# Kernel tuning notes

Hardware: AMD Instinct MI355X
Metric: run time of the kernel (lower is better)

Reference implementation:

```python
import jax, jax.numpy as jnp
import numpy as np

D_MODEL, D_K, D_V, HEAD = 512, 512, 512, 8
SCALE = 1.0 / np.sqrt(D_K)  # torch code divides by sqrt(d_k) (full d_k, not head_dim)
NEG = -1.0e9


def setup_inputs() -> dict:
    key = jax.random.key(0)
    ks = jax.random.split(key, 10)
    B, S = 2, 4096
    x = jax.random.normal(ks[0], (B, S, D_MODEL), dtype=jnp.float32)
    mask = jax.random.randint(ks[1], (B, S), 0, 2, dtype=jnp.int32)
    s = 1.0 / np.sqrt(D_MODEL)
    Wq = jax.random.normal(ks[2], (D_MODEL, D_K), dtype=jnp.float32) * s
    bq = jnp.zeros((D_K,), jnp.float32)
    Wk = jax.random.normal(ks[3], (D_MODEL, D_K), dtype=jnp.float32) * s
    bk = jnp.zeros((D_K,), jnp.float32)
    Wv = jax.random.normal(ks[4], (D_MODEL, D_V), dtype=jnp.float32) * s
    bv = jnp.zeros((D_V,), jnp.float32)
    Wo = jax.random.normal(ks[5], (D_V, D_MODEL), dtype=jnp.float32) * s
    bo = jnp.zeros((D_MODEL,), jnp.float32)
    return {"x": x, "mask": mask, "Wq": Wq, "bq": bq, "Wk": Wk, "bk": bk,
            "Wv": Wv, "bv": bv, "Wo": Wo, "bo": bo}


def reference(x, mask, Wq, bq, Wk, bk, Wv, bv, Wo, bo):
    B, S, _ = x.shape
    hd_k = D_K // HEAD
    hd_v = D_V // HEAD
    # projections -> [B, H, S, hd]
    Q = (x @ Wq + bq).reshape(B, S, HEAD, hd_k).transpose(0, 2, 1, 3)
    K = (x @ Wk + bk).reshape(B, S, HEAD, hd_k).transpose(0, 2, 1, 3)
    V = (x @ Wv + bv).reshape(B, S, HEAD, hd_v).transpose(0, 2, 1, 3)
    # scores [B, H, S, S], scaled by 1/sqrt(d_k) (full d_k, faithful to source)
    scores = jnp.einsum('bhqd,bhkd->bhqk', Q, K) * SCALE
    m = (mask == 1)[:, None, None, :]  # [B,1,1,S]
    scores = jnp.where(m, NEG, scores)
    attn = jax.nn.softmax(scores, axis=-1)
    out = jnp.einsum('bhqk,bhkd->bhqd', attn, V)  # [B,H,S,hd_v]
    out = out.transpose(0, 2, 1, 3).reshape(B, S, D_V)
    return out @ Wo + bo
```

## Files before the change

kernel.cpp:

```cpp
#include <hip/hip_runtime.h>
#include <hip/hip_bf16.h>
#include <stdint.h>

typedef __attribute__((ext_vector_type(8))) short bf16x8;
typedef __attribute__((ext_vector_type(4))) float f32x4;
typedef __attribute__((ext_vector_type(16))) float f32x16;
typedef __attribute__((ext_vector_type(4))) unsigned int u32x4;

#define MFMA16(a, b, c) __builtin_amdgcn_mfma_f32_16x16x32_bf16(a, b, c, 0, 0, 0)
#define MFMA32(a, b, c) __builtin_amdgcn_mfma_f32_32x32x16_bf16(a, b, c, 0, 0, 0)

constexpr float QSCALE = 0.04419417382415922f * 1.4426950408889634f;

__device__ __forceinline__ void gload_lds16(const void* g, void* l) {
  __builtin_amdgcn_global_load_lds((const __attribute__((address_space(1))) uint32_t*)g,
                                   (__attribute__((address_space(3))) uint32_t*)l, 16, 0, 0);
}
__device__ __forceinline__ bf16x8 lds_read_swz(const short* base, int row, int ch) {
  return *(const bf16x8*)((const char*)base + row * 128 + (((ch ^ row) & 7) << 4));
}
__device__ __forceinline__ short f2b(float f) {
  __hip_bfloat16 h = __float2bfloat16(f);
  return *reinterpret_cast<short*>(&h);
}
__device__ __forceinline__ float exp2fast(float x) {
#if __has_builtin(__builtin_amdgcn_exp2f)
  return __builtin_amdgcn_exp2f(x);
#else
  return exp2f(x);
#endif
}

__global__ void k_cvt_x(const float* __restrict__ x, short* __restrict__ xb) {
  const int i = blockIdx.x * 256 + threadIdx.x;
  const float4 v = ((const float4*)x)[i];
  short4 o;
  o.x = f2b(v.x); o.y = f2b(v.y); o.z = f2b(v.z); o.w = f2b(v.w);
  ((short4*)xb)[i] = o;
}

__global__ void k_cvt_w(const float* __restrict__ wq, const float* __restrict__ wk,
                        const float* __restrict__ wv, const float* __restrict__ wo,
                        short* __restrict__ wt) {
  __shared__ float tile[64][65];
  const int mat = blockIdx.x >> 6;
  const int t6 = blockIdx.x & 63;
  const int k0 = (t6 >> 3) * 64, n0 = (t6 & 7) * 64;
  const float* w = (mat == 0) ? wq : (mat == 1) ? wk : (mat == 2) ? wv : wo;
  const int c = threadIdx.x & 63, r4 = threadIdx.x >> 6;
#pragma unroll
  for (int p = 0; p < 16; ++p) {
    const int r = p * 4 + r4;
    tile[r][c] = w[(k0 + r) * 512 + n0 + c];
  }
  __syncthreads();
#pragma unroll
  for (int p = 0; p < 16; ++p) {
    const int r = p * 4 + r4;
    wt[mat * 262144 + (n0 + r) * 512 + k0 + c] = f2b(tile[c][r]);
  }
}

__global__ void k_scan(const int* __restrict__ mask, int* __restrict__ perm,
                       int* __restrict__ cnt) {
  __shared__ int ws[16];
  const int b = blockIdx.x, tid = threadIdx.x;
  const int lane = tid & 63, w = tid >> 6;
  const int* m = mask + b * 4096;
  int v[4], s = 0;
#pragma unroll
  for (int j = 0; j < 4; ++j) { v[j] = (m[tid * 4 + j] == 0) ? 1 : 0; s += v[j]; }
  int sc = s;
  for (int d = 1; d < 64; d <<= 1) { int t = __shfl_up(sc, d); if (lane >= d) sc += t; }
  if (lane == 63) ws[w] = sc;
  __syncthreads();
  if (tid == 0) {
    int acc = 0;
    for (int i = 0; i < 16; ++i) { int t = ws[i]; ws[i] = acc; acc += t; }
    cnt[b] = acc;
  }
  __syncthreads();
  int pos = ws[w] + sc - s;
  int* p = perm + b * 4096;
#pragma unroll
  for (int j = 0; j < 4; ++j) { p[tid * 4 + j] = v[j] ? pos : -1; pos += v[j]; }
}

__global__ __launch_bounds__(256, 2) void k_gemmqkv(
    const short* __restrict__ A, const short* __restrict__ W,
    const float* __restrict__ bq, const float* __restrict__ bk,
    const float* __restrict__ bv, const int* __restrict__ perm,
    short* __restrict__ oq, short* __restrict__ ok, short* __restrict__ ov) {
  __shared__ short Asm[2][128 * 64];
  __shared__ short Bsm[2][128 * 64];
  const int tid = threadIdx.x;
  const int wave = tid >> 6, lane = tid & 63;
  const int lane15 = lane & 15, g = lane >> 4;
  const int wm = wave >> 1, wn = wave & 1;
  const int m0 = blockIdx.x * 128;
  const int n0 = blockIdx.y * 128;

  const char* Ag = (const char*)A + (size_t)m0 * 1024;
  const char* Bg = (const char*)W + (size_t)n0 * 1024;

  f32x4 acc[4][4] = {};

  auto stage = [&](int buf, int kt) {
    const int k0b = kt * 128;
#pragma unroll
    for (int q = 0; q < 4; ++q) {
      int s_ = (wave * 4 + q) * 64 + lane;
      int row = s_ >> 3, ch = s_ & 7;
      gload_lds16(Ag + (size_t)row * 1024 + k0b + (((ch ^ row) & 7) << 4),
                  (char*)&Asm[buf][0] + s_ * 16);
      gload_lds16(Bg + (size_t)row * 1024 + k0b + (((ch ^ row) & 7) << 4),
                  (char*)&Bsm[buf][0] + s_ * 16);
    }
  };

  stage(0, 0);
  asm volatile("s_waitcnt vmcnt(0)" ::: "memory");
  __syncthreads();

  for (int kt = 0; kt < 8; ++kt) {
    const int cur = kt & 1;
    if (kt < 7) stage(cur ^ 1, kt + 1);
#pragma unroll
    for (int kk = 0; kk < 2; ++kk) {
      bf16x8 af[4], bfr[4];
#pragma unroll
      for (int m = 0; m < 4; ++m)
        af[m] = lds_read_swz(&Asm[cur][0], wm * 64 + m * 16 + lane15, kk * 4 + g);
#pragma unroll
      for (int n = 0; n < 4; ++n)
        bfr[n] = lds_read_swz(&Bsm[cur][0], wn * 64 + n * 16 + lane15, kk * 4 + g);
      __builtin_amdgcn_s_setprio(1);
#pragma unroll
      for (int m = 0; m < 4; ++m)
#pragma unroll
        for (int n = 0; n < 4; ++n)
          acc[m][n] = MFMA16(bfr[n], af[m], acc[m][n]);
      __builtin_amdgcn_s_setprio(0);
    }
    asm volatile("s_waitcnt vmcnt(0)" ::: "memory");
    __syncthreads();
  }

  const int mat = blockIdx.y >> 2;
  const float* bptr = (mat == 0) ? bq : (mat == 1) ? bk : bv;
  const int hh = ((n0 & 511) >> 6) + wn;
  const int hb = g >> 1, j4 = (g & 1) * 4;

#pragma unroll
  for (int mf = 0; mf < 4; ++mf) {
    const int rowg = m0 + wm * 64 + mf * 16 + lane15;
    const int b_ = rowg >> 12, sl = rowg & 4095;
    const size_t bh = (size_t)(b_ * 8 + hh);
    int pm_ = 0;
    if (mat != 0) pm_ = perm[b_ * 4096 + sl];
#pragma unroll
    for (int nf = 0; nf < 4; ++nf) {
      const int nn = (n0 & 511) + wn * 64 + nf * 16 + g * 4;
      const float4 b4 = *(const float4*)(bptr + nn);
      const float v0 = acc[mf][nf][0] + b4.x;
      const float v1 = acc[mf][nf][1] + b4.y;
      const float v2 = acc[mf][nf][2] + b4.z;
      const float v3 = acc[mf][nf][3] + b4.w;
      if (mat == 0) {
        short4 s4;
        s4.x = f2b(v0 * QSCALE); s4.y = f2b(v1 * QSCALE);
        s4.z = f2b(v2 * QSCALE); s4.w = f2b(v3 * QSCALE);
        *(short4*)(oq + bh * 262144 +
                   (size_t)(((sl >> 5) * 4 + nf) * 64 + hb * 32 + (sl & 31)) * 8 + j4) = s4;
      } else if (pm_ >= 0) {
        const int t = pm_ >> 6, r = pm_ & 63;
        if (mat == 1) {
          short4 s4;
          s4.x = f2b(v0); s4.y = f2b(v1); s4.z = f2b(v2); s4.w = f2b(v3);
          *(short4*)(ok + bh * 262144 +
                     (size_t)((t * 8 + nf * 2 + (r >> 5)) * 64 + hb * 32 + (r & 31)) * 8 + j4) = s4;
        } else {
          const int mm = (r & ~12) | (((r >> 2) & 1) << 3) | (((r >> 3) & 1) << 2);
          short* base = ov + bh * 262144 +
                        (size_t)((t * 8 + ((mm >> 4) & 3) * 2 + (nf >> 1)) * 64 +
                                 ((mm >> 3) & 1) * 32 + (nf & 1) * 16 + g * 4) * 8 + (mm & 7);
          base[0] = f2b(v0); base[8] = f2b(v1); base[16] = f2b(v2); base[24] = f2b(v3);
        }
      }
    }
  }
}

__global__ __launch_bounds__(256, 2) void k_gemmo(
    const short* __restrict__ A, const short* __restrict__ W,
    const float* __restrict__ bias, float* __restrict__ fo) {
  __shared__ short Asm[2][128 * 64];
  __shared__ short Bsm[2][64 * 64];
  const int tid = threadIdx.x;
  const int wave = tid >> 6, lane = tid & 63;
  const int lane15 = lane & 15, g = lane >> 4;
  const int wm = wave >> 1, wn = wave & 1;
  const int m0 = blockIdx.x * 128;
  const int n0 = blockIdx.y * 64;

  const char* Ag = (const char*)A + (size_t)m0 * 1024;
  const char* Bg = (const char*)W + (size_t)n0 * 1024;

  f32x4 acc[4][2] = {};

  auto stage = [&](int buf, int kt) {
    const int k0b = kt * 128;
#pragma unroll
    for (int q = 0; q < 4; ++q) {
      int s_ = (wave * 4 + q) * 64 + lane;
      int row = s_ >> 3, ch = s_ & 7;
      gload_lds16(Ag + (size_t)row * 1024 + k0b + (((ch ^ row) & 7) << 4),
                  (char*)&Asm[buf][0] + s_ * 16);
    }
#pragma unroll
    for (int q = 0; q < 2; ++q) {
      int s_ = (wave * 2 + q) * 64 + lane;
      int row = s_ >> 3, ch = s_ & 7;
      gload_lds16(Bg + (size_t)row * 1024 + k0b + (((ch ^ row) & 7) << 4),
                  (char*)&Bsm[buf][0] + s_ * 16);
    }
  };

  stage(0, 0);
  asm volatile("s_waitcnt vmcnt(0)" ::: "memory");
  __syncthreads();

  for (int kt = 0; kt < 8; ++kt) {
    const int cur = kt & 1;
    if (kt < 7) stage(cur ^ 1, kt + 1);
#pragma unroll
    for (int kk = 0; kk < 2; ++kk) {
      bf16x8 af[4], bfr[2];
#pragma unroll
      for (int m = 0; m < 4; ++m)
        af[m] = lds_read_swz(&Asm[cur][0], wm * 64 + m * 16 + lane15, kk * 4 + g);
#pragma unroll
      for (int n = 0; n < 2; ++n)
        bfr[n] = lds_read_swz(&Bsm[cur][0], wn * 32 + n * 16 + lane15, kk * 4 + g);
      __builtin_amdgcn_s_setprio(1);
#pragma unroll
      for (int m = 0; m < 4; ++m)
#pragma unroll
        for (int n = 0; n < 2; ++n)
          acc[m][n] = MFMA16(bfr[n], af[m], acc[m][n]);
      __builtin_amdgcn_s_setprio(0);
    }
    asm volatile("s_waitcnt vmcnt(0)" ::: "memory");
    __syncthreads();
  }

#pragma unroll
  for (int mf = 0; mf < 4; ++mf) {
    const int rowg = m0 + wm * 64 + mf * 16 + lane15;
#pragma unroll
    for (int nf = 0; nf < 2; ++nf) {
      const int cb = n0 + wn * 32 + nf * 16 + g * 4;
      const float4 b4 = *(const float4*)(bias + cb);
      float4 o4;
      o4.x = acc[mf][nf][0] + b4.x;
      o4.y = acc[mf][nf][1] + b4.y;
      o4.z = acc[mf][nf][2] + b4.z;
      o4.w = acc[mf][nf][3] + b4.w;
      *(float4*)(fo + (size_t)rowg * 512 + cb) = o4;
    }
  }
}

__global__ __launch_bounds__(256, 2) void k_attn(
    const short* __restrict__ Qp, const short* __restrict__ Kp,
    const short* __restrict__ Vp, const int* __restrict__ cnt,
    short* __restrict__ out) {
  __shared__ short Ks[2][8][512];
  __shared__ short Vs[2][8][512];

  const int tid = threadIdx.x;
  const int wave = tid >> 6, lane = tid & 63;
  const int l31 = lane & 31, h = lane >> 5;
  const int bid = blockIdx.x;
  const int sid = (bid & 7) * 64 + (bid >> 3);
  const int qt = sid & 31, bh = sid >> 5;
  const int b = bh >> 3, hh = bh & 7;
  const int qb = qt * 4 + wave;

  const short* Qg = Qp + (size_t)bh * 262144;
  const short* Kg = Kp + (size_t)bh * 262144;
  const short* Vg = Vp + (size_t)bh * 262144;

  bf16x8 qreg[4];
#pragma unroll
  for (int dk = 0; dk < 4; ++dk)
    qreg[dk] = *(const bf16x8*)(Qg + ((size_t)(qb * 4 + dk) * 64 + lane) * 8);

  const int cn = cnt[b];
  const int nt = max(1, (cn + 63) >> 6);
  const int lim = cn - (nt - 1) * 64;

  auto stage = [&](int buf, int t) {
#pragma unroll
    for (int q = 0; q < 2; ++q) {
      const int u = wave * 2 + q;
      gload_lds16(Kg + ((size_t)(t * 8 + u) * 64 + lane) * 8, &Ks[buf][u][lane * 8]);
      gload_lds16(Vg + ((size_t)(t * 8 + u) * 64 + lane) * 8, &Vs[buf][u][lane * 8]);
    }
  };
  auto ldsK = [&](int buf, int u) { return *(const bf16x8*)&Ks[buf][u][lane * 8]; };
  auto ldsV = [&](int buf, int u) { return *(const bf16x8*)&Vs[buf][u][lane * 8]; };

  f32x16 o0 = {}, o1 = {};
  float l_ = 0.f;

  stage(0, 0);
  __syncthreads();

  for (int t = 0; t < nt; ++t) {
    const int cur = t & 1;
    if (t + 1 < nt) stage(cur ^ 1, t + 1);

    f32x16 s0v = {}, s1v = {};
    __builtin_amdgcn_s_setprio(1);
#pragma unroll
    for (int dk = 0; dk < 4; ++dk) {
      s0v = MFMA32(ldsK(cur, 2 * dk), qreg[dk], s0v);
      s1v = MFMA32(ldsK(cur, 2 * dk + 1), qreg[dk], s1v);
    }
    __builtin_amdgcn_s_setprio(0);

    if (t == nt - 1 && lim < 64) {
#pragma unroll
      for (int i = 0; i < 16; ++i) {
        const int r0 = (i & 3) + 8 * (i >> 2) + 4 * h;
        if (r0 >= lim) s0v[i] = -1e30f;
        if (r0 + 32 >= lim) s1v[i] = -1e30f;
      }
    }

    unsigned int wA[8], wB[8];
    float ts = 0.f;
#pragma unroll
    for (int j2 = 0; j2 < 8; ++j2) {
      float a0 = exp2fast(s0v[2 * j2]);
      float a1 = exp2fast(s0v[2 * j2 + 1]);
      float b0 = exp2fast(s1v[2 * j2]);
      float b1 = exp2fast(s1v[2 * j2 + 1]);
      ts += (a0 + a1) + (b0 + b1);
      asm("v_cvt_pk_bf16_f32 %0, %1, %2" : "=v"(wA[j2]) : "v"(a0), "v"(a1));
      asm("v_cvt_pk_bf16_f32 %0, %1, %2" : "=v"(wB[j2]) : "v"(b0), "v"(b1));
    }
    l_ += ts;

    __builtin_amdgcn_s_setprio(1);
#pragma unroll
    for (int s = 0; s < 4; ++s) {
      const bf16x8 v0 = ldsV(cur, 2 * s);
      const bf16x8 v1 = ldsV(cur, 2 * s + 1);
      const unsigned int* w = (s < 2) ? wA : wB;
      union PU { u32x4 u; bf16x8 f; } pu;
      pu.u[0] = w[4 * (s & 1) + 0];
      pu.u[1] = w[4 * (s & 1) + 1];
      pu.u[2] = w[4 * (s & 1) + 2];
      pu.u[3] = w[4 * (s & 1) + 3];
      o0 = MFMA32(v0, pu.f, o0);
      o1 = MFMA32(v1, pu.f, o1);
    }
    __builtin_amdgcn_s_setprio(0);

    __syncthreads();
  }

  l_ += __shfl_xor(l_, 32);
  const float inv = 1.0f / l_;
  short* og = out + (size_t)(b * 4096 + qb * 32 + l31) * 512 + hh * 64;
#pragma unroll
  for (int r2 = 0; r2 < 4; ++r2) {
    {
      const int base = 8 * r2 + 4 * h;
      short4 s4;
      s4.x = f2b(o0[4 * r2 + 0] * inv);
      s4.y = f2b(o0[4 * r2 + 1] * inv);
      s4.z = f2b(o0[4 * r2 + 2] * inv);
      s4.w = f2b(o0[4 * r2 + 3] * inv);
      *(short4*)(og + base) = s4;
    }
    {
      const int base = 32 + 8 * r2 + 4 * h;
      short4 s4;
      s4.x = f2b(o1[4 * r2 + 0] * inv);
      s4.y = f2b(o1[4 * r2 + 1] * inv);
      s4.z = f2b(o1[4 * r2 + 2] * inv);
      s4.w = f2b(o1[4 * r2 + 3] * inv);
      *(short4*)(og + base) = s4;
    }
  }
}

extern "C" void kernel_launch(void* const* d_in, const int* in_sizes, int n_in,
                              void* d_out, int out_size, void* d_ws, size_t ws_size,
                              hipStream_t stream) {
  const float* x  = (const float*)d_in[0];
  const int* mask = (const int*)d_in[1];
  const float* Wq = (const float*)d_in[2];
  const float* bq = (const float*)d_in[3];
  const float* Wk = (const float*)d_in[4];
  const float* bk = (const float*)d_in[5];
  const float* Wv = (const float*)d_in[6];
  const float* bv = (const float*)d_in[7];
  const float* Wo = (const float*)d_in[8];
  const float* bo = (const float*)d_in[9];
  float* out = (float*)d_out;

  short* xb   = (short*)d_ws;
  short* wt   = xb + (size_t)8192 * 512;
  short* qws  = wt + (size_t)4 * 512 * 512;
  short* kws  = qws + (size_t)8192 * 512;
  short* vws  = kws + (size_t)8192 * 512;
  short* aout = vws + (size_t)8192 * 512;
  int* perm   = (int*)(aout + (size_t)8192 * 512);
  int* cntw   = perm + 8192;

  k_cvt_x<<<4096, 256, 0, stream>>>(x, xb);
  k_cvt_w<<<256, 256, 0, stream>>>(Wq, Wk, Wv, Wo, wt);
  k_scan<<<2, 1024, 0, stream>>>(mask, perm, cntw);
  k_gemmqkv<<<dim3(64, 12), 256, 0, stream>>>(xb, wt, bq, bk, bv, perm, qws, kws, vws);
  k_attn<<<512, 256, 0, stream>>>(qws, kws, vws, cntw, aout);
  k_gemmo<<<dim3(64, 8), 256, 0, stream>>>(aout, wt + (size_t)3 * 512 * 512, bo, out);
}
```

Before: 166.9 us.

## Merge prep kernels into one launch and process two KV tiles per attention iteration

Three preprocessing kernels (x conversion, weight transpose, mask scan) are folded into a single launch, with block-index ranges selecting each job, to save two launch gaps. The attention loop now stages and processes two 64-key tiles per iteration using doubled LDS buffers and separate accumulators. This halves the barrier count and gives the scheduler more independent MFMA and exp work to interleave. The cost is double the LDS footprint, which may limit occupancy, and higher register pressure. When the tile count is odd it also loads and masks one extra padded tile.

```diff
diff --git a/kernel.cpp b/kernel.cpp
--- a/kernel.cpp
+++ b/kernel.cpp
@@ -31,59 +31,62 @@
 #endif
 }
 
-__global__ void k_cvt_x(const float* __restrict__ x, short* __restrict__ xb) {
-  const int i = blockIdx.x * 256 + threadIdx.x;
-  const float4 v = ((const float4*)x)[i];
-  short4 o;
-  o.x = f2b(v.x); o.y = f2b(v.y); o.z = f2b(v.z); o.w = f2b(v.w);
-  ((short4*)xb)[i] = o;
-}
-
-__global__ void k_cvt_w(const float* __restrict__ wq, const float* __restrict__ wk,
-                        const float* __restrict__ wv, const float* __restrict__ wo,
-                        short* __restrict__ wt) {
+__global__ void k_prep(const float* __restrict__ x,
+                       const float* __restrict__ wq, const float* __restrict__ wk,
+                       const float* __restrict__ wv, const float* __restrict__ wo,
+                       const int* __restrict__ mask,
+                       short* __restrict__ xb, short* __restrict__ wt,
+                       int* __restrict__ perm, int* __restrict__ cnt) {
   __shared__ float tile[64][65];
-  const int mat = blockIdx.x >> 6;
-  const int t6 = blockIdx.x & 63;
-  const int k0 = (t6 >> 3) * 64, n0 = (t6 & 7) * 64;
-  const float* w = (mat == 0) ? wq : (mat == 1) ? wk : (mat == 2) ? wv : wo;
-  const int c = threadIdx.x & 63, r4 = threadIdx.x >> 6;
-#pragma unroll
-  for (int p = 0; p < 16; ++p) {
-    const int r = p * 4 + r4;
-    tile[r][c] = w[(k0 + r) * 512 + n0 + c];
-  }
-  __syncthreads();
-#pragma unroll
-  for (int p = 0; p < 16; ++p) {
-    const int r = p * 4 + r4;
-    wt[mat * 262144 + (n0 + r) * 512 + k0 + c] = f2b(tile[c][r]);
-  }
-}
-
-__global__ void k_scan(const int* __restrict__ mask, int* __restrict__ perm,
-                       int* __restrict__ cnt) {
-  __shared__ int ws[16];
-  const int b = blockIdx.x, tid = threadIdx.x;
-  const int lane = tid & 63, w = tid >> 6;
-  const int* m = mask + b * 4096;
-  int v[4], s = 0;
-#pragma unroll
-  for (int j = 0; j < 4; ++j) { v[j] = (m[tid * 4 + j] == 0) ? 1 : 0; s += v[j]; }
-  int sc = s;
-  for (int d = 1; d < 64; d <<= 1) { int t = __shfl_up(sc, d); if (lane >= d) sc += t; }
-  if (lane == 63) ws[w] = sc;
-  __syncthreads();
-  if (tid == 0) {
-    int acc = 0;
-    for (int i = 0; i < 16; ++i) { int t = ws[i]; ws[i] = acc; acc += t; }
-    cnt[b] = acc;
-  }
-  __syncthreads();
-  int pos = ws[w] + sc - s;
-  int* p = perm + b * 4096;
-#pragma unroll
-  for (int j = 0; j < 4; ++j) { p[tid * 4 + j] = v[j] ? pos : -1; pos += v[j]; }
+  __shared__ int ws4[4];
+  const int bid = blockIdx.x, tid = threadIdx.x;
+
+  if (bid < 4096) {
+    const int i = bid * 256 + tid;
+    const float4 v = ((const float4*)x)[i];
+    short4 o;
+    o.x = f2b(v.x); o.y = f2b(v.y); o.z = f2b(v.z); o.w = f2b(v.w);
+    ((short4*)xb)[i] = o;
+  } else if (bid < 4352) {
+    const int bp = bid - 4096;
+    const int mat = bp >> 6;
+    const int t6 = bp & 63;
+    const int k0 = (t6 >> 3) * 64, n0 = (t6 & 7) * 64;
+    const float* w = (mat == 0) ? wq : (mat == 1) ? wk : (mat == 2) ? wv : wo;
+    const int c = tid & 63, r4 = tid >> 6;
+#pragma unroll
+    for (int p = 0; p < 16; ++p) {
+      const int r = p * 4 + r4;
+      tile[r][c] = w[(k0 + r) * 512 + n0 + c];
+    }
+    __syncthreads();
+#pragma unroll
+    for (int p = 0; p < 16; ++p) {
+      const int r = p * 4 + r4;
+      wt[mat * 262144 + (n0 + r) * 512 + k0 + c] = f2b(tile[c][r]);
+    }
+  } else {
+    const int b = bid - 4352;
+    const int lane = tid & 63, w = tid >> 6;
+    const int* m = mask + b * 4096;
+    int v[16], s = 0;
+#pragma unroll
+    for (int j = 0; j < 16; ++j) { v[j] = (m[tid * 16 + j] == 0) ? 1 : 0; s += v[j]; }
+    int sc = s;
+    for (int d = 1; d < 64; d <<= 1) { int t = __shfl_up(sc, d); if (lane >= d) sc += t; }
+    if (lane == 63) ws4[w] = sc;
+    __syncthreads();
+    if (tid == 0) {
+      int acc = 0;
+      for (int i = 0; i < 4; ++i) { int t = ws4[i]; ws4[i] = acc; acc += t; }
+      cnt[b] = acc;
+    }
+    __syncthreads();
+    int pos = ws4[w] + sc - s;
+    int* p = perm + b * 4096;
+#pragma unroll
+    for (int j = 0; j < 16; ++j) { p[tid * 16 + j] = v[j] ? pos : -1; pos += v[j]; }
+  }
 }
 
 __global__ __launch_bounds__(256, 2) void k_gemmqkv(
@@ -275,8 +278,8 @@
     const short* __restrict__ Qp, const short* __restrict__ Kp,
     const short* __restrict__ Vp, const int* __restrict__ cnt,
     short* __restrict__ out) {
-  __shared__ short Ks[2][8][512];
-  __shared__ short Vs[2][8][512];
+  __shared__ short Ks[2][2][8][512];
+  __shared__ short Vs[2][2][8][512];
 
   const int tid = threadIdx.x;
   const int wave = tid >> 6, lane = tid & 63;
@@ -298,80 +301,128 @@
 
   const int cn = cnt[b];
   const int nt = max(1, (cn + 63) >> 6);
-  const int lim = cn - (nt - 1) * 64;
-
-  auto stage = [&](int buf, int t) {
+  const int ntp = (nt + 1) >> 1;
+
+  auto stage = [&](int buf, int tp) {
 #pragma unroll
     for (int q = 0; q < 2; ++q) {
       const int u = wave * 2 + q;
-      gload_lds16(Kg + ((size_t)(t * 8 + u) * 64 + lane) * 8, &Ks[buf][u][lane * 8]);
-      gload_lds16(Vg + ((size_t)(t * 8 + u) * 64 + lane) * 8, &Vs[buf][u][lane * 8]);
+#pragma unroll
+      for (int tt = 0; tt < 2; ++tt) {
+        const int t = tp * 2 + tt;
+        gload_lds16(Kg + ((size_t)(t * 8 + u) * 64 + lane) * 8, &Ks[buf][tt][u][lane * 8]);
+        gload_lds16(Vg + ((size_t)(t * 8 + u) * 64 + lane) * 8, &Vs[buf][tt][u][lane * 8]);
+      }
     }
   };
-  auto ldsK = [&](int buf, int u) { return *(const bf16x8*)&Ks[buf][u][lane * 8]; };
-  auto ldsV = [&](int buf, int u) { return *(const bf16x8*)&Vs[buf][u][lane * 8]; };
-
-  f32x16 o0 = {}, o1 = {};
+  auto ldsK = [&](int buf, int tt, int u) { return *(const bf16x8*)&Ks[buf][tt][u][lane * 8]; };
+  auto ldsV = [&](int buf, int tt, int u) { return *(const bf16x8*)&Vs[buf][tt][u][lane * 8]; };
+
+  f32x16 o0a = {}, o0b = {}, o1a = {}, o1b = {};
   float l_ = 0.f;
 
   stage(0, 0);
   __syncthreads();
 
-  for (int t = 0; t < nt; ++t) {
-    const int cur = t & 1;
-    if (t + 1 < nt) stage(cur ^ 1, t + 1);
-
-    f32x16 s0v = {}, s1v = {};
+  for (int tp = 0; tp < ntp; ++tp) {
+    const int cur = tp & 1;
+    if (tp + 1 < ntp) stage(cur ^ 1, tp + 1);
+
+    f32x16 sA0 = {}, sA1 = {}, sB0 = {}, sB1 = {};
     __builtin_amdgcn_s_setprio(1);
 #pragma unroll
     for (int dk = 0; dk < 4; ++dk) {
-      s0v = MFMA32(ldsK(cur, 2 * dk), qreg[dk], s0v);
-      s1v = MFMA32(ldsK(cur, 2 * dk + 1), qreg[dk], s1v);
+      sA0 = MFMA32(ldsK(cur, 0, 2 * dk), qreg[dk], sA0);
+      sA1 = MFMA32(ldsK(cur, 0, 2 * dk + 1), qreg[dk], sA1);
+    }
+#pragma unroll
+    for (int dk = 0; dk < 4; ++dk) {
+      sB0 = MFMA32(ldsK(cur, 1, 2 * dk), qreg[dk], sB0);
+      sB1 = MFMA32(ldsK(cur, 1, 2 * dk + 1), qreg[dk], sB1);
     }
     __builtin_amdgcn_s_setprio(0);
 
-    if (t == nt - 1 && lim < 64) {
+    const int lim0 = cn - (tp * 2) * 64;
+    const int lim1 = cn - (tp * 2 + 1) * 64;
+    if (lim0 < 64) {
 #pragma unroll
       for (int i = 0; i < 16; ++i) {
         const int r0 = (i & 3) + 8 * (i >> 2) + 4 * h;
-        if (r0 >= lim) s0v[i] = -1e30f;
-        if (r0 + 32 >= lim) s1v[i] = -1e30f;
+        if (r0 >= lim0) sA0[i] = -1e30f;
+        if (r0 + 32 >= lim0) sA1[i] = -1e30f;
       }
     }
-
-    unsigned int wA[8], wB[8];
-    float ts = 0.f;
+    if (lim1 < 64) {
+#pragma unroll
+      for (int i = 0; i < 16; ++i) {
+        const int r0 = (i & 3) + 8 * (i >> 2) + 4 * h;
+        if (r0 >= lim1) sB0[i] = -1e30f;
+        if (r0 + 32 >= lim1) sB1[i] = -1e30f;
+      }
+    }
+
+    unsigned int w00[8], w01[8];
+    float ts0 = 0.f;
 #pragma unroll
     for (int j2 = 0; j2 < 8; ++j2) {
-      float a0 = exp2fast(s0v[2 * j2]);
-      float a1 = exp2fast(s0v[2 * j2 + 1]);
-      float b0 = exp2fast(s1v[2 * j2]);
-      float b1 = exp2fast(s1v[2 * j2 + 1]);
-      ts += (a0 + a1) + (b0 + b1);
-      asm("v_cvt_pk_bf16_f32 %0, %1, %2" : "=v"(wA[j2]) : "v"(a0), "v"(a1));
-      asm("v_cvt_pk_bf16_f32 %0, %1, %2" : "=v"(wB[j2]) : "v"(b0), "v"(b1));
-    }
-    l_ += ts;
-
+      float a0 = exp2fast(sA0[2 * j2]);
+      float a1 = exp2fast(sA0[2 * j2 + 1]);
+      float b0 = exp2fast(sA1[2 * j2]);
+      float b1 = exp2fast(sA1[2 * j2 + 1]);
+      ts0 += (a0 + a1) + (b0 + b1);
+      asm("v_cvt_pk_bf16_f32 %0, %1, %2" : "=v"(w00[j2]) : "v"(a0), "v"(a1));
+      asm("v_cvt_pk_bf16_f32 %0, %1, %2" : "=v"(w01[j2]) : "v"(b0), "v"(b1));
+    }
     __builtin_amdgcn_s_setprio(1);
 #pragma unroll
     for (int s = 0; s < 4; ++s) {
-      const bf16x8 v0 = ldsV(cur, 2 * s);
-      const bf16x8 v1 = ldsV(cur, 2 * s + 1);
-      const unsigned int* w = (s < 2) ? wA : wB;
+      const bf16x8 v0 = ldsV(cur, 0, 2 * s);
+      const bf16x8 v1 = ldsV(cur, 0, 2 * s + 1);
+      const unsigned int* w = (s < 2) ? w00 : w01;
       union PU { u32x4 u; bf16x8 f; } pu;
       pu.u[0] = w[4 * (s & 1) + 0];
       pu.u[1] = w[4 * (s & 1) + 1];
       pu.u[2] = w[4 * (s & 1) + 2];
       pu.u[3] = w[4 * (s & 1) + 3];
-      o0 = MFMA32(v0, pu.f, o0);
-      o1 = MFMA32(v1, pu.f, o1);
+      o0a = MFMA32(v0, pu.f, o0a);
+      o1a = MFMA32(v1, pu.f, o1a);
     }
     __builtin_amdgcn_s_setprio(0);
 
-    __syncthreads();
-  }
-
+    unsigned int w10[8], w11[8];
+    float ts1 = 0.f;
+#pragma unroll
+    for (int j2 = 0; j2 < 8; ++j2) {
+      float a0 = exp2fast(sB0[2 * j2]);
+      float a1 = exp2fast(sB0[2 * j2 + 1]);
+      float b0 = exp2fast(sB1[2 * j2]);
+      float b1 = exp2fast(sB1[2 * j2 + 1]);
+      ts1 += (a0 + a1) + (b0 + b1);
+      asm("v_cvt_pk_bf16_f32 %0, %1, %2" : "=v"(w10[j2]) : "v"(a0), "v"(a1));
+      asm("v_cvt_pk_bf16_f32 %0, %1, %2" : "=v"(w11[j2]) : "v"(b0), "v"(b1));
+    }
+    l_ += ts0 + ts1;
+    __builtin_amdgcn_s_setprio(1);
+#pragma unroll
+    for (int s = 0; s < 4; ++s) {
+      const bf16x8 v0 = ldsV(cur, 1, 2 * s);
+      const bf16x8 v1 = ldsV(cur, 1, 2 * s + 1);
+      const unsigned int* w = (s < 2) ? w10 : w11;
+      union PU { u32x4 u; bf16x8 f; } pu;
+      pu.u[0] = w[4 * (s & 1) + 0];
+      pu.u[1] = w[4 * (s & 1) + 1];
+      pu.u[2] = w[4 * (s & 1) + 2];
+      pu.u[3] = w[4 * (s & 1) + 3];
+      o0b = MFMA32(v0, pu.f, o0b);
+      o1b = MFMA32(v1, pu.f, o1b);
+    }
+    __builtin_amdgcn_s_setprio(0);
+
+    __syncthreads();
+  }
+
+  const f32x16 o0 = o0a + o0b;
+  const f32x16 o1 = o1a + o1b;
   l_ += __shfl_xor(l_, 32);
   const float inv = 1.0f / l_;
   short* og = out + (size_t)(b * 4096 + qb * 32 + l31) * 512 + hh * 64;
@@ -422,9 +473,7 @@
   int* perm   = (int*)(aout + (size_t)8192 * 512);
   int* cntw   = perm + 8192;
 
-  k_cvt_x<<<4096, 256, 0, stream>>>(x, xb);
-  k_cvt_w<<<256, 256, 0, stream>>>(Wq, Wk, Wv, Wo, wt);
-  k_scan<<<2, 1024, 0, stream>>>(mask, perm, cntw);
+  k_prep<<<4354, 256, 0, stream>>>(x, Wq, Wk, Wv, Wo, mask, xb, wt, perm, cntw);
   k_gemmqkv<<<dim3(64, 12), 256, 0, stream>>>(xb, wt, bq, bk, bv, perm, qws, kws, vws);
   k_attn<<<512, 256, 0, stream>>>(qws, kws, vws, cntw, aout);
   k_gemmo<<<dim3(64, 8), 256, 0, stream>>>(aout, wt + (size_t)3 * 512 * 512, bo, out);
```

Measured after the change: 163.9 us. Within noise of the previous version (-1.8%).

## Deepen attention K/V prefetch to four slots and fuse prep kernels

Applied to the files above, without the earlier changes.

The attention kernel moves from a double buffer to a four-slot LDS ring. It prefetches two tiles ahead, waits with a partial vmcnt and uses one barrier per iteration instead of two sync points. The PV accumulation is split across two accumulator pairs, which shortens MFMA dependency chains, and the mask check is made per tile. The three preprocessing kernels (x cast, weight transpose, mask scan) are merged into one launch, and s_setprio is dropped from both GEMMs. This doubles the attention LDS footprint and issues a few redundant loads of the last tile.

```diff
diff --git a/kernel.cpp b/kernel.cpp
--- a/kernel.cpp
+++ b/kernel.cpp
@@ -31,59 +31,62 @@
 #endif
 }
 
-__global__ void k_cvt_x(const float* __restrict__ x, short* __restrict__ xb) {
-  const int i = blockIdx.x * 256 + threadIdx.x;
-  const float4 v = ((const float4*)x)[i];
-  short4 o;
-  o.x = f2b(v.x); o.y = f2b(v.y); o.z = f2b(v.z); o.w = f2b(v.w);
-  ((short4*)xb)[i] = o;
-}
-
-__global__ void k_cvt_w(const float* __restrict__ wq, const float* __restrict__ wk,
-                        const float* __restrict__ wv, const float* __restrict__ wo,
-                        short* __restrict__ wt) {
+__global__ void k_prep(const float* __restrict__ x,
+                       const float* __restrict__ wq, const float* __restrict__ wk,
+                       const float* __restrict__ wv, const float* __restrict__ wo,
+                       const int* __restrict__ mask,
+                       short* __restrict__ xb, short* __restrict__ wt,
+                       int* __restrict__ perm, int* __restrict__ cnt) {
   __shared__ float tile[64][65];
-  const int mat = blockIdx.x >> 6;
-  const int t6 = blockIdx.x & 63;
-  const int k0 = (t6 >> 3) * 64, n0 = (t6 & 7) * 64;
-  const float* w = (mat == 0) ? wq : (mat == 1) ? wk : (mat == 2) ? wv : wo;
-  const int c = threadIdx.x & 63, r4 = threadIdx.x >> 6;
-#pragma unroll
-  for (int p = 0; p < 16; ++p) {
-    const int r = p * 4 + r4;
-    tile[r][c] = w[(k0 + r) * 512 + n0 + c];
-  }
-  __syncthreads();
-#pragma unroll
-  for (int p = 0; p < 16; ++p) {
-    const int r = p * 4 + r4;
-    wt[mat * 262144 + (n0 + r) * 512 + k0 + c] = f2b(tile[c][r]);
-  }
-}
-
-__global__ void k_scan(const int* __restrict__ mask, int* __restrict__ perm,
-                       int* __restrict__ cnt) {
-  __shared__ int ws[16];
-  const int b = blockIdx.x, tid = threadIdx.x;
-  const int lane = tid & 63, w = tid >> 6;
-  const int* m = mask + b * 4096;
-  int v[4], s = 0;
-#pragma unroll
-  for (int j = 0; j < 4; ++j) { v[j] = (m[tid * 4 + j] == 0) ? 1 : 0; s += v[j]; }
-  int sc = s;
-  for (int d = 1; d < 64; d <<= 1) { int t = __shfl_up(sc, d); if (lane >= d) sc += t; }
-  if (lane == 63) ws[w] = sc;
-  __syncthreads();
-  if (tid == 0) {
-    int acc = 0;
-    for (int i = 0; i < 16; ++i) { int t = ws[i]; ws[i] = acc; acc += t; }
-    cnt[b] = acc;
-  }
-  __syncthreads();
-  int pos = ws[w] + sc - s;
-  int* p = perm + b * 4096;
-#pragma unroll
-  for (int j = 0; j < 4; ++j) { p[tid * 4 + j] = v[j] ? pos : -1; pos += v[j]; }
+  __shared__ int ws4[4];
+  const int bid = blockIdx.x, tid = threadIdx.x;
+
+  if (bid < 4096) {
+    const int i = bid * 256 + tid;
+    const float4 v = ((const float4*)x)[i];
+    short4 o;
+    o.x = f2b(v.x); o.y = f2b(v.y); o.z = f2b(v.z); o.w = f2b(v.w);
+    ((short4*)xb)[i] = o;
+  } else if (bid < 4352) {
+    const int bp = bid - 4096;
+    const int mat = bp >> 6;
+    const int t6 = bp & 63;
+    const int k0 = (t6 >> 3) * 64, n0 = (t6 & 7) * 64;
+    const float* w = (mat == 0) ? wq : (mat == 1) ? wk : (mat == 2) ? wv : wo;
+    const int c = tid & 63, r4 = tid >> 6;
+#pragma unroll
+    for (int p = 0; p < 16; ++p) {
+      const int r = p * 4 + r4;
+      tile[r][c] = w[(k0 + r) * 512 + n0 + c];
+    }
+    __syncthreads();
+#pragma unroll
+    for (int p = 0; p < 16; ++p) {
+      const int r = p * 4 + r4;
+      wt[mat * 262144 + (n0 + r) * 512 + k0 + c] = f2b(tile[c][r]);
+    }
+  } else {
+    const int b = bid - 4352;
+    const int lane = tid & 63, w = tid >> 6;
+    const int* m = mask + b * 4096;
+    int v[16], s = 0;
+#pragma unroll
+    for (int j = 0; j < 16; ++j) { v[j] = (m[tid * 16 + j] == 0) ? 1 : 0; s += v[j]; }
+    int sc = s;
+    for (int d = 1; d < 64; d <<= 1) { int t = __shfl_up(sc, d); if (lane >= d) sc += t; }
+    if (lane == 63) ws4[w] = sc;
+    __syncthreads();
+    if (tid == 0) {
+      int acc = 0;
+      for (int i = 0; i < 4; ++i) { int t = ws4[i]; ws4[i] = acc; acc += t; }
+      cnt[b] = acc;
+    }
+    __syncthreads();
+    int pos = ws4[w] + sc - s;
+    int* p = perm + b * 4096;
+#pragma unroll
+    for (int j = 0; j < 16; ++j) { p[tid * 16 + j] = v[j] ? pos : -1; pos += v[j]; }
+  }
 }
 
 __global__ __launch_bounds__(256, 2) void k_gemmqkv(
@@ -134,13 +137,11 @@
 #pragma unroll
       for (int n = 0; n < 4; ++n)
         bfr[n] = lds_read_swz(&Bsm[cur][0], wn * 64 + n * 16 + lane15, kk * 4 + g);
-      __builtin_amdgcn_s_setprio(1);
 #pragma unroll
       for (int m = 0; m < 4; ++m)
 #pragma unroll
         for (int n = 0; n < 4; ++n)
           acc[m][n] = MFMA16(bfr[n], af[m], acc[m][n]);
-      __builtin_amdgcn_s_setprio(0);
     }
     asm volatile("s_waitcnt vmcnt(0)" ::: "memory");
     __syncthreads();
@@ -242,13 +243,11 @@
 #pragma unroll
       for (int n = 0; n < 2; ++n)
         bfr[n] = lds_read_swz(&Bsm[cur][0], wn * 32 + n * 16 + lane15, kk * 4 + g);
-      __builtin_amdgcn_s_setprio(1);
 #pragma unroll
       for (int m = 0; m < 4; ++m)
 #pragma unroll
         for (int n = 0; n < 2; ++n)
           acc[m][n] = MFMA16(bfr[n], af[m], acc[m][n]);
-      __builtin_amdgcn_s_setprio(0);
     }
     asm volatile("s_waitcnt vmcnt(0)" ::: "memory");
     __syncthreads();
@@ -275,8 +274,8 @@
     const short* __restrict__ Qp, const short* __restrict__ Kp,
     const short* __restrict__ Vp, const int* __restrict__ cnt,
     short* __restrict__ out) {
-  __shared__ short Ks[2][8][512];
-  __shared__ short Vs[2][8][512];
+  __shared__ short Ks[4][8][512];
+  __shared__ short Vs[4][8][512];
 
   const int tid = threadIdx.x;
   const int wave = tid >> 6, lane = tid & 63;
@@ -298,28 +297,31 @@
 
   const int cn = cnt[b];
   const int nt = max(1, (cn + 63) >> 6);
-  const int lim = cn - (nt - 1) * 64;
-
-  auto stage = [&](int buf, int t) {
+
+  auto stage = [&](int slot, int t) {
 #pragma unroll
     for (int q = 0; q < 2; ++q) {
       const int u = wave * 2 + q;
-      gload_lds16(Kg + ((size_t)(t * 8 + u) * 64 + lane) * 8, &Ks[buf][u][lane * 8]);
-      gload_lds16(Vg + ((size_t)(t * 8 + u) * 64 + lane) * 8, &Vs[buf][u][lane * 8]);
+      gload_lds16(Kg + ((size_t)(t * 8 + u) * 64 + lane) * 8, &Ks[slot][u][lane * 8]);
+      gload_lds16(Vg + ((size_t)(t * 8 + u) * 64 + lane) * 8, &Vs[slot][u][lane * 8]);
     }
   };
-  auto ldsK = [&](int buf, int u) { return *(const bf16x8*)&Ks[buf][u][lane * 8]; };
-  auto ldsV = [&](int buf, int u) { return *(const bf16x8*)&Vs[buf][u][lane * 8]; };
-
-  f32x16 o0 = {}, o1 = {};
+  auto ldsK = [&](int slot, int u) { return *(const bf16x8*)&Ks[slot][u][lane * 8]; };
+  auto ldsV = [&](int slot, int u) { return *(const bf16x8*)&Vs[slot][u][lane * 8]; };
+
+  f32x16 o0x = {}, o0y = {}, o1x = {}, o1y = {};
   float l_ = 0.f;
 
   stage(0, 0);
-  __syncthreads();
+  stage(1, min(1, nt - 1));
 
   for (int t = 0; t < nt; ++t) {
-    const int cur = t & 1;
-    if (t + 1 < nt) stage(cur ^ 1, t + 1);
+    const int cur = t & 3;
+    stage((t + 2) & 3, min(t + 2, nt - 1));
+    asm volatile("s_waitcnt vmcnt(8)" ::: "memory");
+    __builtin_amdgcn_sched_barrier(0);
+    __builtin_amdgcn_s_barrier();
+    __builtin_amdgcn_sched_barrier(0);
 
     f32x16 s0v = {}, s1v = {};
     __builtin_amdgcn_s_setprio(1);
@@ -330,7 +332,8 @@
     }
     __builtin_amdgcn_s_setprio(0);
 
-    if (t == nt - 1 && lim < 64) {
+    const int lim = cn - t * 64;
+    if (lim < 64) {
 #pragma unroll
       for (int i = 0; i < 16; ++i) {
         const int r0 = (i & 3) + 8 * (i >> 2) + 4 * h;
@@ -364,14 +367,19 @@
       pu.u[1] = w[4 * (s & 1) + 1];
       pu.u[2] = w[4 * (s & 1) + 2];
       pu.u[3] = w[4 * (s & 1) + 3];
-      o0 = MFMA32(v0, pu.f, o0);
-      o1 = MFMA32(v1, pu.f, o1);
+      if (s & 1) {
+        o0y = MFMA32(v0, pu.f, o0y);
+        o1y = MFMA32(v1, pu.f, o1y);
+      } else {
+        o0x = MFMA32(v0, pu.f, o0x);
+        o1x = MFMA32(v1, pu.f, o1x);
+      }
     }
     __builtin_amdgcn_s_setprio(0);
-
-    __syncthreads();
-  }
-
+  }
+
+  const f32x16 o0 = o0x + o0y;
+  const f32x16 o1 = o1x + o1y;
   l_ += __shfl_xor(l_, 32);
   const float inv = 1.0f / l_;
   short* og = out + (size_t)(b * 4096 + qb * 32 + l31) * 512 + hh * 64;
@@ -422,9 +430,7 @@
   int* perm   = (int*)(aout + (size_t)8192 * 512);
   int* cntw   = perm + 8192;
 
-  k_cvt_x<<<4096, 256, 0, stream>>>(x, xb);
-  k_cvt_w<<<256, 256, 0, stream>>>(Wq, Wk, Wv, Wo, wt);
-  k_scan<<<2, 1024, 0, stream>>>(mask, perm, cntw);
+  k_prep<<<4354, 256, 0, stream>>>(x, Wq, Wk, Wv, Wo, mask, xb, wt, perm, cntw);
   k_gemmqkv<<<dim3(64, 12), 256, 0, stream>>>(xb, wt, bq, bk, bv, perm, qws, kws, vws);
   k_attn<<<512, 256, 0, stream>>>(qws, kws, vws, cntw, aout);
   k_gemmo<<<dim3(64, 8), 256, 0, stream>>>(aout, wt + (size_t)3 * 512 * 512, bo, out);
```

New measurement: 162.8 us. 2.5% less time.
